# Optimization experiments

Hardware: AMD Instinct MI355X
Metric: run time of the kernel (lower is better)

Reference implementation:

```python
import jax, jax.numpy as jnp
import numpy as np

D_MODEL = 1024
NUM_HEADS = 16
D_K = D_MODEL // NUM_HEADS
B, L = 2, 2048


def setup_inputs() -> dict:
    key = jax.random.key(0)
    ks = jax.random.split(key, 10)
    s = 1.0 / np.sqrt(D_MODEL)
    inp = {
        "x": jax.random.normal(ks[0], (B, L, D_MODEL), dtype=jnp.float32),
        "mask": jnp.ones((B, L, L), dtype=jnp.int32),
        "wq": jax.random.uniform(ks[1], (D_MODEL, D_MODEL), jnp.float32, -s, s),
        "bq": jax.random.uniform(ks[2], (D_MODEL,), jnp.float32, -s, s),
        "wk": jax.random.uniform(ks[3], (D_MODEL, D_MODEL), jnp.float32, -s, s),
        "bk": jax.random.uniform(ks[4], (D_MODEL,), jnp.float32, -s, s),
        "wv": jax.random.uniform(ks[5], (D_MODEL, D_MODEL), jnp.float32, -s, s),
        "bv": jax.random.uniform(ks[6], (D_MODEL,), jnp.float32, -s, s),
        "wo": jax.random.uniform(ks[7], (D_MODEL, D_MODEL), jnp.float32, -s, s),
        "bo": jax.random.uniform(ks[8], (D_MODEL,), jnp.float32, -s, s),
    }
    return inp


def reference(x, mask, wq, bq, wk, bk, wv, bv, wo, bo):
    Bs, Ls, C = x.shape
    # linear projections, then split heads: [B, L, C] -> [B, h, L, d_k]
    def split_heads(t):
        return t.reshape(Bs, Ls, NUM_HEADS, D_K).transpose(0, 2, 1, 3)
    q = split_heads(x @ wq + bq)
    k = split_heads(x @ wk + bk)
    v = split_heads(x @ wv + bv)
    scores = jnp.einsum("bhlc,bhkc->bhlk", q, k) / np.sqrt(D_K)
    # mask: [B, L, L] -> [B, 1, L, L]; fill masked positions with -1e9
    scores = jnp.where(mask[:, None, :, :] == 0, jnp.float32(-1e9), scores)
    attn = jax.nn.softmax(scores, axis=-1)  # dropout p=0.0 -> identity
    out = jnp.einsum("bhlk,bhkc->bhlc", attn, v)
    out = out.transpose(0, 2, 1, 3).reshape(Bs, Ls, C)
    return out @ wo + bo
```

## Files before the change

kernel.cpp:

```cpp
#include <hip/hip_runtime.h>
#include <stdint.h>

#define D_MODEL 1024
#define NHEAD   16
#define DK      64
#define BATCH   2
#define SEQ     2048
#define MTOT    (BATCH*SEQ)

typedef unsigned short u16;
typedef unsigned int   u32;
typedef u16    u16x4  __attribute__((ext_vector_type(4)));
typedef u16    u16x8  __attribute__((ext_vector_type(8)));
typedef u32    u32x4  __attribute__((ext_vector_type(4)));
typedef __bf16 bf16x8 __attribute__((ext_vector_type(8)));
typedef float  f32x4  __attribute__((ext_vector_type(4)));
typedef float  f32x16 __attribute__((ext_vector_type(16)));

__device__ __forceinline__ u16 f2bf(float f) {
  union { float f; unsigned u; } v; v.f = f;
  return (u16)((v.u + 0x7fffu + ((v.u >> 16) & 1u)) >> 16);
}

__device__ __forceinline__ void gl_lds16(const void* g, void* l) {
  __builtin_amdgcn_global_load_lds((const __attribute__((address_space(1))) void*)g,
                                   (__attribute__((address_space(3))) void*)l, 16, 0, 0);
}

__device__ __forceinline__ bf16x8 ld_frag(const u16* p) {
  return __builtin_bit_cast(bf16x8, *(const u16x8*)p);
}

__device__ __forceinline__ u32 cvtpk(float lo, float hi) {
  u32 r;
  asm("v_cvt_pk_bf16_f32 %0, %1, %2" : "=v"(r) : "v"(lo), "v"(hi));
  return r;
}

__global__ __launch_bounds__(256) void k_cvt_x(const float* __restrict__ x, u16* __restrict__ xb) {
  int i = blockIdx.x * 256 + threadIdx.x;
  const float4 v = ((const float4*)x)[i];
  u16x4 o; o[0]=f2bf(v.x); o[1]=f2bf(v.y); o[2]=f2bf(v.z); o[3]=f2bf(v.w);
  *(u16x4*)(xb + (size_t)i*4) = o;
}

__global__ __launch_bounds__(256) void k_wtrans(const float* __restrict__ wq, const float* __restrict__ wk,
                                                const float* __restrict__ wv, const float* __restrict__ wo,
                                                u16* __restrict__ wqkv_t, u16* __restrict__ wo_t) {
  __shared__ float tile[32][33];
  const int z = blockIdx.z;
  const float* src = (z==0)?wq:(z==1)?wk:(z==2)?wv:wo;
  const int kb = blockIdx.y*32, nb = blockIdx.x*32;
  const int tx = threadIdx.x & 31, ty = threadIdx.x >> 5;
  #pragma unroll
  for (int i=0;i<4;i++)
    tile[ty + i*8][tx] = src[(size_t)(kb + ty + i*8)*D_MODEL + nb + tx];
  __syncthreads();
  u16* dst = (z<3) ? (wqkv_t + (size_t)z*D_MODEL*D_MODEL) : wo_t;
  #pragma unroll
  for (int i=0;i<4;i++) {
    int n = nb + ty + i*8, k = kb + tx;
    dst[(size_t)n*D_MODEL + k] = f2bf(tile[tx][ty + i*8]);
  }
}

__global__ __launch_bounds__(256) void k_maskpack(const int* __restrict__ mask,
                                                  unsigned long long* __restrict__ mb) {
  const int wid = blockIdx.x*4 + (threadIdx.x >> 6);
  const int lane = threadIdx.x & 63;
  for (int t2 = 0; t2 < 32; ++t2) {
    int word = wid*32 + t2;
    int row = word >> 5;
    int kb = word & 31;
    int m = mask[(size_t)row*SEQ + kb*64 + lane];
    unsigned long long bits = __ballot(m != 0);
    if (lane == 0) mb[word] = bits;
  }
}

__global__ __launch_bounds__(256) void k_vtrans(const u16* __restrict__ V, u16* __restrict__ Vt) {
  __shared__ u16 tile[64][72];
  const int bh = blockIdx.x >> 5;
  const int l0 = (blockIdx.x & 31) * 64;
  const int t = threadIdx.x;
  const u16* src = V + ((size_t)bh*SEQ + l0)*DK;
  #pragma unroll
  for (int j=0;j<2;j++) {
    int idx = t + j*256;
    int r = idx >> 3, c8 = (idx & 7)*8;
    *(u16x8*)&tile[r][c8] = *(const u16x8*)(src + (size_t)r*DK + c8);
  }
  __syncthreads();
  u16* dst = Vt + (size_t)bh*DK*SEQ + l0;
  #pragma unroll
  for (int j=0;j<2;j++) {
    int idx = t + j*256;
    int d = idx >> 3, k8 = (idx & 7)*8;
    u16x8 o;
    #pragma unroll
    for (int e=0;e<8;e++) o[e] = tile[k8 + e][d];
    *(u16x8*)(dst + (size_t)d*SEQ + k8) = o;
  }
}

template<int EPI>
__global__ __launch_bounds__(256) void k_gemm(const u16* __restrict__ A, const u16* __restrict__ Bt,
                                              const int M, const int N, const int K, const int nbm,
                                              const float* __restrict__ bq, const float* __restrict__ bk,
                                              const float* __restrict__ bv,
                                              u16* __restrict__ Qo, u16* __restrict__ Ko, u16* __restrict__ Vo,
                                              const float* __restrict__ bo, float* __restrict__ out) {
  __shared__ u16 As[128*32];
  __shared__ u16 Bs[128*32];
  const int t = threadIdx.x, lane = t & 63, w = t >> 6;
  const int bm = blockIdx.x % nbm, bn = blockIdx.x / nbm;
  const int brow = bm*128, bcol = bn*128;

  const int srow = w*32 + (lane >> 2);
  const int sswz = (lane & 3) ^ ((lane >> 2) & 3);
  const u16* aS0 = A  + (size_t)(brow + srow)*K + sswz*8;
  const u16* aS1 = aS0 + (size_t)16*K;
  const u16* bS0 = Bt + (size_t)(bcol + srow)*K + sswz*8;
  const u16* bS1 = bS0 + (size_t)16*K;
  u16* aD0 = As + w*1024; u16* aD1 = aD0 + 512;
  u16* bD0 = Bs + w*1024; u16* bD1 = bD0 + 512;

  const int wr = w >> 1, wc = w & 1;
  const int slotA = (lane >> 4) ^ (lane & 3);
  const u16* aRd = As + (wr*64 + (lane & 15))*32 + slotA*8;
  const u16* bRd = Bs + (wc*64 + (lane & 15))*32 + slotA*8;

  f32x4 acc[4][4];
  #pragma unroll
  for (int i=0;i<4;i++)
    #pragma unroll
    for (int j=0;j<4;j++) acc[i][j] = (f32x4){0.f,0.f,0.f,0.f};

  for (int kt = 0; kt < K; kt += 32) {
    gl_lds16(aS0 + kt, aD0);
    gl_lds16(aS1 + kt, aD1);
    gl_lds16(bS0 + kt, bD0);
    gl_lds16(bS1 + kt, bD1);
    __syncthreads();
    bf16x8 af[4], bfr[4];
    #pragma unroll
    for (int m=0;m<4;m++) af[m] = ld_frag(aRd + m*512);
    #pragma unroll
    for (int n=0;n<4;n++) bfr[n] = ld_frag(bRd + n*512);
    #pragma unroll
    for (int m=0;m<4;m++)
      #pragma unroll
      for (int n=0;n<4;n++)
        acc[m][n] = __builtin_amdgcn_mfma_f32_16x16x32_bf16(af[m], bfr[n], acc[m][n], 0,0,0);
    __syncthreads();
  }

  const int orow = brow + wr*64 + (lane >> 4)*4;
  const int ocol = bcol + wc*64 + (lane & 15);
  if (EPI == 0) {
    const int mat = ocol >> 10;
    const float* bias = (mat==0) ? bq : (mat==1) ? bk : bv;
    u16* outp = (mat==0) ? Qo : (mat==1) ? Ko : Vo;
    const float scal = (mat==0) ? 0.125f*1.4426950408889634f : 1.0f;
    #pragma unroll
    for (int m=0;m<4;m++) {
      #pragma unroll
      for (int n=0;n<4;n++) {
        int col = ocol + n*16;
        int c = col & 1023;
        float bb = bias[c];
        int h = c >> 6, d = c & 63;
        #pragma unroll
        for (int j=0;j<4;j++) {
          int row = orow + m*16 + j;
          int b = row >> 11, l = row & 2047;
          float v = (acc[m][n][j] + bb) * scal;
          outp[(((size_t)(b*NHEAD + h)*SEQ + l) << 6) + d] = f2bf(v);
        }
      }
    }
  } else {
    #pragma unroll
    for (int m=0;m<4;m++)
      #pragma unroll
      for (int n=0;n<4;n++) {
        int col = ocol + n*16;
        float bb = bo[col];
        #pragma unroll
        for (int j=0;j<4;j++) {
          int row = orow + m*16 + j;
          out[(size_t)row*N + col] = acc[m][n][j] + bb;
        }
      }
  }
}

__global__ __launch_bounds__(512, 4) void k_attn(const u16* __restrict__ Q, const u16* __restrict__ K,
                                                 const u16* __restrict__ Vt,
                                                 const unsigned long long* __restrict__ MB,
                                                 u16* __restrict__ AO) {
  __shared__ char smem[36864];
  const int t = threadIdx.x, lane = t & 63, w = t >> 6;
  const int hf = w >> 2, widx = w & 3;
  const int bid = blockIdx.x;
  const int swz = (bid & 7)*64 + (bid >> 3);
  const int bh = swz >> 4;
  const int q0 = (swz & 15) * 128;
  const int b = bh >> 4, h = bh & 15;
  const int lq = lane & 31, hi = lane >> 5, l7 = lane & 7;

  u16* Kbuf = (u16*)(smem + hf*16384);
  u16* Vbuf = (u16*)(smem + hf*16384 + 8192);

  const int qg = q0 + widx*32 + lq;
  const u16* qp = Q + ((size_t)bh*SEQ + qg)*DK + hi*8;
  bf16x8 qf[4];
  #pragma unroll
  for (int ks=0;ks<4;ks++) qf[ks] = ld_frag(qp + ks*16);

  const int srow = widx*16 + (lane >> 3);
  const int sswz = l7 ^ ((lane >> 3) & 7);
  const u16* kSb = K  + ((size_t)bh*SEQ + srow)*DK + sswz*8;
  const u16* vSb = Vt + ((size_t)bh*DK + srow)*SEQ + sswz*8;
  u16* kD0 = Kbuf + widx*1024; u16* kD1 = kD0 + 512;
  u16* vD0 = Vbuf + widx*1024; u16* vD1 = vD0 + 512;

  f32x16 o0 = 0.f, o1 = 0.f;
  float m_run = -1e30f, l_run = 0.f;
  const unsigned long long* mbp = MB + ((size_t)b*SEQ + qg)*32;

  for (int i = 0; i < 16; ++i) {
    const int ktg = hf*16 + i;
    const u16* kp = kSb + (size_t)ktg*64*DK;
    const u16* vp = vSb + ktg*64;
    gl_lds16(kp, kD0); gl_lds16(kp + 8*DK, kD1);
    gl_lds16(vp, vD0); gl_lds16(vp + 8*SEQ, vD1);
    __syncthreads();

    f32x16 s0 = 0.f, s1 = 0.f;
    #pragma unroll
    for (int ks=0;ks<4;ks++) {
      const int ph = (ks*2 + hi) ^ l7;
      bf16x8 kf0 = ld_frag(Kbuf + lq*64 + ph*8);
      bf16x8 kf1 = ld_frag(Kbuf + (32+lq)*64 + ph*8);
      s0 = __builtin_amdgcn_mfma_f32_32x32x16_bf16(kf0, qf[ks], s0, 0,0,0);
      s1 = __builtin_amdgcn_mfma_f32_32x32x16_bf16(kf1, qf[ks], s1, 0,0,0);
    }

    unsigned long long mb = mbp[ktg];
    if (!__all(mb == ~0ull)) {
      #pragma unroll
      for (int r=0;r<16;r++) {
        int kl = (r&3) + 8*(r>>2) + 4*hi;
        if (!((mb >> kl) & 1ull)) s0[r] = -1e9f;
        if (!((mb >> (kl+32)) & 1ull)) s1[r] = -1e9f;
      }
    }

    float tm[16];
    #pragma unroll
    for (int r=0;r<16;r++) tm[r] = fmaxf(s0[r], s1[r]);
    #pragma unroll
    for (int st=8; st>0; st>>=1)
      #pragma unroll
      for (int r=0;r<8;r++) if (r < st) tm[r] = fmaxf(tm[r], tm[r+st]);
    float mx = fmaxf(tm[0], __shfl_xor(tm[0], 32));
    if (!__all(mx <= m_run + 8.0f)) {
      float m_new = fmaxf(m_run, mx);
      float corr = __builtin_amdgcn_exp2f(m_run - m_new);
      l_run *= corr;
      #pragma unroll
      for (int r=0;r<16;r++) { o0[r] *= corr; o1[r] *= corr; }
      m_run = m_new;
    }
    float ts[16];
    #pragma unroll
    for (int r=0;r<16;r++) {
      s0[r] = __builtin_amdgcn_exp2f(s0[r] - m_run);
      s1[r] = __builtin_amdgcn_exp2f(s1[r] - m_run);
      ts[r] = s0[r] + s1[r];
    }
    #pragma unroll
    for (int st=8; st>0; st>>=1)
      #pragma unroll
      for (int r=0;r<8;r++) if (r < st) ts[r] += ts[r+st];
    l_run += ts[0] + __shfl_xor(ts[0], 32);

    #pragma unroll
    for (int kt2=0;kt2<2;kt2++) {
      const f32x16& sv = kt2 ? s1 : s0;
      u32 w0 = cvtpk(sv[0],  sv[1]),  w1 = cvtpk(sv[2],  sv[3]);
      u32 w2 = cvtpk(sv[4],  sv[5]),  w3 = cvtpk(sv[6],  sv[7]);
      u32 w4 = cvtpk(sv[8],  sv[9]),  w5 = cvtpk(sv[10], sv[11]);
      u32 w6 = cvtpk(sv[12], sv[13]), w7 = cvtpk(sv[14], sv[15]);
      asm volatile("v_permlane32_swap_b32 %0, %1" : "+v"(w0), "+v"(w2));
      asm volatile("v_permlane32_swap_b32 %0, %1" : "+v"(w1), "+v"(w3));
      asm volatile("v_permlane32_swap_b32 %0, %1" : "+v"(w4), "+v"(w6));
      asm volatile("v_permlane32_swap_b32 %0, %1" : "+v"(w5), "+v"(w7));
      bf16x8 pa0 = __builtin_bit_cast(bf16x8, (u32x4){w0, w1, w2, w3});
      bf16x8 pa1 = __builtin_bit_cast(bf16x8, (u32x4){w4, w5, w6, w7});
      const int ph0 = ((kt2*2+0)*2 + hi) ^ l7;
      const int ph1 = ((kt2*2+1)*2 + hi) ^ l7;
      bf16x8 v00 = ld_frag(Vbuf + lq*64      + ph0*8);
      bf16x8 v01 = ld_frag(Vbuf + lq*64      + ph1*8);
      bf16x8 v10 = ld_frag(Vbuf + (32+lq)*64 + ph0*8);
      bf16x8 v11 = ld_frag(Vbuf + (32+lq)*64 + ph1*8);
      o0 = __builtin_amdgcn_mfma_f32_32x32x16_bf16(v00, pa0, o0, 0,0,0);
      o0 = __builtin_amdgcn_mfma_f32_32x32x16_bf16(v01, pa1, o0, 0,0,0);
      o1 = __builtin_amdgcn_mfma_f32_32x32x16_bf16(v10, pa0, o1, 0,0,0);
      o1 = __builtin_amdgcn_mfma_f32_32x32x16_bf16(v11, pa1, o1, 0,0,0);
    }
    __syncthreads();
  }

  float* marea = (float*)smem;
  if (hf == 1) {
    float* p = marea + (size_t)(widx*64 + lane)*35;
    #pragma unroll
    for (int r=0;r<16;r++) { p[r] = o0[r]; p[16+r] = o1[r]; }
    p[32] = m_run; p[33] = l_run;
  }
  __syncthreads();
  if (hf == 0) {
    const float* p = marea + (size_t)(widx*64 + lane)*35;
    float m1 = p[32], l1 = p[33];
    float mm = fmaxf(m_run, m1);
    float c0 = __builtin_amdgcn_exp2f(m_run - mm);
    float c1 = __builtin_amdgcn_exp2f(m1 - mm);
    float inv = 1.0f / (l_run*c0 + l1*c1);
    size_t base = ((size_t)(b*SEQ + qg))*D_MODEL + h*DK;
    u16x4 g;
    #pragma unroll
    for (int rr=0;rr<4;rr++) {
      #pragma unroll
      for (int i2=0;i2<4;i2++) g[i2] = f2bf((o0[rr*4+i2]*c0 + p[rr*4+i2]*c1) * inv);
      *(u16x4*)(AO + base + rr*8 + hi*4) = g;
    }
    #pragma unroll
    for (int rr=0;rr<4;rr++) {
      #pragma unroll
      for (int i2=0;i2<4;i2++) g[i2] = f2bf((o1[rr*4+i2]*c0 + p[16+rr*4+i2]*c1) * inv);
      *(u16x4*)(AO + base + 32 + rr*8 + hi*4) = g;
    }
  }
}

extern "C" void kernel_launch(void* const* d_in, const int* in_sizes, int n_in,
                              void* d_out, int out_size, void* d_ws, size_t ws_size,
                              hipStream_t stream) {
  const float* x  = (const float*)d_in[0];
  const int*  msk = (const int*)d_in[1];
  const float* wq = (const float*)d_in[2];
  const float* bq = (const float*)d_in[3];
  const float* wk = (const float*)d_in[4];
  const float* bk = (const float*)d_in[5];
  const float* wv = (const float*)d_in[6];
  const float* bv = (const float*)d_in[7];
  const float* wo = (const float*)d_in[8];
  const float* bo = (const float*)d_in[9];
  float* out = (float*)d_out;

  char* ws = (char*)d_ws;
  size_t off = 0;
  u16* Xb   = (u16*)(ws + off); off += (size_t)MTOT*D_MODEL*2;
  u16* Wqkv = (u16*)(ws + off); off += (size_t)3*D_MODEL*D_MODEL*2;
  u16* Wot  = (u16*)(ws + off); off += (size_t)D_MODEL*D_MODEL*2;
  u16* Qb   = (u16*)(ws + off); off += (size_t)BATCH*NHEAD*SEQ*DK*2;
  u16* Kb   = (u16*)(ws + off); off += (size_t)BATCH*NHEAD*SEQ*DK*2;
  u16* Vb   = (u16*)(ws + off); off += (size_t)BATCH*NHEAD*SEQ*DK*2;
  u16* Vtb  = (u16*)(ws + off); off += (size_t)BATCH*NHEAD*SEQ*DK*2;
  u16* AO   = (u16*)(ws + off); off += (size_t)MTOT*D_MODEL*2;
  unsigned long long* Mb = (unsigned long long*)(ws + off);

  k_cvt_x<<<MTOT*D_MODEL/4/256, 256, 0, stream>>>(x, Xb);
  k_wtrans<<<dim3(32,32,4), 256, 0, stream>>>(wq, wk, wv, wo, Wqkv, Wot);
  k_maskpack<<<1024, 256, 0, stream>>>(msk, Mb);
  k_gemm<0><<<(MTOT/128)*(3*D_MODEL/128), 256, 0, stream>>>(
      Xb, Wqkv, MTOT, 3*D_MODEL, D_MODEL, MTOT/128,
      bq, bk, bv, Qb, Kb, Vb, nullptr, nullptr);
  k_vtrans<<<BATCH*NHEAD*(SEQ/64), 256, 0, stream>>>(Vb, Vtb);
  k_attn<<<BATCH*NHEAD*(SEQ/128), 512, 0, stream>>>(Qb, Kb, Vtb, Mb, AO);
  k_gemm<1><<<(MTOT/128)*(D_MODEL/128), 256, 0, stream>>>(
      AO, Wot, MTOT, D_MODEL, D_MODEL, MTOT/128,
      nullptr, nullptr, nullptr, nullptr, nullptr, nullptr, bo, out);
}
```

Measured before the change: 151.7 us.

## Double-buffer K/V tiles in LDS and split softmax into 32-key sub-blocks

The attention kernel now double-buffers K and V tiles in LDS, prefetching the next tile with async global-to-LDS loads while the current one is computed. This replaces the two per-iteration __syncthreads with a single waitcnt plus barrier. The 64-key tile is now handled as two 32-key sub-blocks with an online softmax update per sub-block, which lowers register pressure. MFMA sections are wrapped in s_setprio. LDS use grows from 36KB to 64KB per block, which cuts blocks per CU and may hurt occupancy against launch_bounds(512,4).

```diff
diff --git a/kernel.cpp b/kernel.cpp
--- a/kernel.cpp
+++ b/kernel.cpp
@@ -199,7 +199,7 @@
                                                  const u16* __restrict__ Vt,
                                                  const unsigned long long* __restrict__ MB,
                                                  u16* __restrict__ AO) {
-  __shared__ char smem[36864];
+  __shared__ char smem[65536];
   const int t = threadIdx.x, lane = t & 63, w = t >> 6;
   const int hf = w >> 2, widx = w & 3;
   const int bid = blockIdx.x;
@@ -209,9 +209,6 @@
   const int b = bh >> 4, h = bh & 15;
   const int lq = lane & 31, hi = lane >> 5, l7 = lane & 7;
 
-  u16* Kbuf = (u16*)(smem + hf*16384);
-  u16* Vbuf = (u16*)(smem + hf*16384 + 8192);
-
   const int qg = q0 + widx*32 + lq;
   const u16* qp = Q + ((size_t)bh*SEQ + qg)*DK + hi*8;
   bf16x8 qf[4];
@@ -222,96 +219,107 @@
   const int sswz = l7 ^ ((lane >> 3) & 7);
   const u16* kSb = K  + ((size_t)bh*SEQ + srow)*DK + sswz*8;
   const u16* vSb = Vt + ((size_t)bh*DK + srow)*SEQ + sswz*8;
-  u16* kD0 = Kbuf + widx*1024; u16* kD1 = kD0 + 512;
-  u16* vD0 = Vbuf + widx*1024; u16* vD1 = vD0 + 512;
 
   f32x16 o0 = 0.f, o1 = 0.f;
   float m_run = -1e30f, l_run = 0.f;
   const unsigned long long* mbp = MB + ((size_t)b*SEQ + qg)*32;
 
+  #define STAGE(buf, tile) do {                                           \
+    const u16* kp_ = kSb + (size_t)(tile)*64*DK;                          \
+    const u16* vp_ = vSb + (size_t)(tile)*64;                             \
+    u16* kd_ = (u16*)(smem + (buf)*32768 + hf*16384) + widx*1024;         \
+    u16* vd_ = (u16*)(smem + (buf)*32768 + hf*16384 + 8192) + widx*1024;  \
+    gl_lds16(kp_, kd_); gl_lds16(kp_ + 8*DK, kd_ + 512);                  \
+    gl_lds16(vp_, vd_); gl_lds16(vp_ + 8*SEQ, vd_ + 512);                 \
+  } while (0)
+
+  STAGE(0, hf*16);
+  asm volatile("s_waitcnt vmcnt(0)" ::: "memory");
+  __builtin_amdgcn_s_barrier();
+
   for (int i = 0; i < 16; ++i) {
-    const int ktg = hf*16 + i;
-    const u16* kp = kSb + (size_t)ktg*64*DK;
-    const u16* vp = vSb + ktg*64;
-    gl_lds16(kp, kD0); gl_lds16(kp + 8*DK, kD1);
-    gl_lds16(vp, vD0); gl_lds16(vp + 8*SEQ, vD1);
-    __syncthreads();
-
-    f32x16 s0 = 0.f, s1 = 0.f;
-    #pragma unroll
-    for (int ks=0;ks<4;ks++) {
-      const int ph = (ks*2 + hi) ^ l7;
-      bf16x8 kf0 = ld_frag(Kbuf + lq*64 + ph*8);
-      bf16x8 kf1 = ld_frag(Kbuf + (32+lq)*64 + ph*8);
-      s0 = __builtin_amdgcn_mfma_f32_32x32x16_bf16(kf0, qf[ks], s0, 0,0,0);
-      s1 = __builtin_amdgcn_mfma_f32_32x32x16_bf16(kf1, qf[ks], s1, 0,0,0);
-    }
-
-    unsigned long long mb = mbp[ktg];
-    if (!__all(mb == ~0ull)) {
-      #pragma unroll
-      for (int r=0;r<16;r++) {
-        int kl = (r&3) + 8*(r>>2) + 4*hi;
-        if (!((mb >> kl) & 1ull)) s0[r] = -1e9f;
-        if (!((mb >> (kl+32)) & 1ull)) s1[r] = -1e9f;
-      }
-    }
-
-    float tm[16];
-    #pragma unroll
-    for (int r=0;r<16;r++) tm[r] = fmaxf(s0[r], s1[r]);
-    #pragma unroll
-    for (int st=8; st>0; st>>=1)
-      #pragma unroll
-      for (int r=0;r<8;r++) if (r < st) tm[r] = fmaxf(tm[r], tm[r+st]);
-    float mx = fmaxf(tm[0], __shfl_xor(tm[0], 32));
-    if (!__all(mx <= m_run + 8.0f)) {
-      float m_new = fmaxf(m_run, mx);
-      float corr = __builtin_amdgcn_exp2f(m_run - m_new);
-      l_run *= corr;
-      #pragma unroll
-      for (int r=0;r<16;r++) { o0[r] *= corr; o1[r] *= corr; }
-      m_run = m_new;
-    }
-    float ts[16];
-    #pragma unroll
-    for (int r=0;r<16;r++) {
-      s0[r] = __builtin_amdgcn_exp2f(s0[r] - m_run);
-      s1[r] = __builtin_amdgcn_exp2f(s1[r] - m_run);
-      ts[r] = s0[r] + s1[r];
-    }
-    #pragma unroll
-    for (int st=8; st>0; st>>=1)
-      #pragma unroll
-      for (int r=0;r<8;r++) if (r < st) ts[r] += ts[r+st];
-    l_run += ts[0] + __shfl_xor(ts[0], 32);
-
-    #pragma unroll
-    for (int kt2=0;kt2<2;kt2++) {
-      const f32x16& sv = kt2 ? s1 : s0;
-      u32 w0 = cvtpk(sv[0],  sv[1]),  w1 = cvtpk(sv[2],  sv[3]);
-      u32 w2 = cvtpk(sv[4],  sv[5]),  w3 = cvtpk(sv[6],  sv[7]);
-      u32 w4 = cvtpk(sv[8],  sv[9]),  w5 = cvtpk(sv[10], sv[11]);
-      u32 w6 = cvtpk(sv[12], sv[13]), w7 = cvtpk(sv[14], sv[15]);
+    const int cur = i & 1;
+    if (i + 1 < 16) STAGE(cur ^ 1, hf*16 + i + 1);
+    const u16* Kbuf = (const u16*)(smem + cur*32768 + hf*16384);
+    const u16* Vbuf = (const u16*)(smem + cur*32768 + hf*16384 + 8192);
+    const unsigned long long mb = mbp[hf*16 + i];
+    const bool full = __all(mb == ~0ull);
+
+    #pragma unroll
+    for (int sub = 0; sub < 2; ++sub) {
+      f32x16 s = 0.f;
+      __builtin_amdgcn_s_setprio(1);
+      #pragma unroll
+      for (int ks=0;ks<4;ks++) {
+        const int ph = (ks*2 + hi) ^ l7;
+        bf16x8 kf = ld_frag(Kbuf + (sub*32 + lq)*64 + ph*8);
+        s = __builtin_amdgcn_mfma_f32_32x32x16_bf16(kf, qf[ks], s, 0,0,0);
+      }
+      __builtin_amdgcn_s_setprio(0);
+
+      if (!full) {
+        #pragma unroll
+        for (int r=0;r<16;r++) {
+          int kl = sub*32 + (r&3) + 8*(r>>2) + 4*hi;
+          if (!((mb >> kl) & 1ull)) s[r] = -1e9f;
+        }
+      }
+
+      float tm[8];
+      #pragma unroll
+      for (int r=0;r<8;r++) tm[r] = fmaxf(s[r], s[8+r]);
+      #pragma unroll
+      for (int st=4; st>0; st>>=1)
+        #pragma unroll
+        for (int r=0;r<4;r++) if (r < st) tm[r] = fmaxf(tm[r], tm[r+st]);
+      float mx = fmaxf(tm[0], __shfl_xor(tm[0], 32));
+      if (!__all(mx <= m_run + 8.0f)) {
+        float m_new = fmaxf(m_run, mx);
+        float corr = __builtin_amdgcn_exp2f(m_run - m_new);
+        l_run *= corr;
+        #pragma unroll
+        for (int r=0;r<16;r++) { o0[r] *= corr; o1[r] *= corr; }
+        m_run = m_new;
+      }
+      #pragma unroll
+      for (int r=0;r<16;r++) s[r] = __builtin_amdgcn_exp2f(s[r] - m_run);
+      float ts[8];
+      #pragma unroll
+      for (int r=0;r<8;r++) ts[r] = s[r] + s[8+r];
+      #pragma unroll
+      for (int st=4; st>0; st>>=1)
+        #pragma unroll
+        for (int r=0;r<4;r++) if (r < st) ts[r] += ts[r+st];
+      l_run += ts[0] + __shfl_xor(ts[0], 32);
+
+      u32 w0 = cvtpk(s[0],  s[1]),  w1 = cvtpk(s[2],  s[3]);
+      u32 w2 = cvtpk(s[4],  s[5]),  w3 = cvtpk(s[6],  s[7]);
+      u32 w4 = cvtpk(s[8],  s[9]),  w5 = cvtpk(s[10], s[11]);
+      u32 w6 = cvtpk(s[12], s[13]), w7 = cvtpk(s[14], s[15]);
       asm volatile("v_permlane32_swap_b32 %0, %1" : "+v"(w0), "+v"(w2));
       asm volatile("v_permlane32_swap_b32 %0, %1" : "+v"(w1), "+v"(w3));
       asm volatile("v_permlane32_swap_b32 %0, %1" : "+v"(w4), "+v"(w6));
       asm volatile("v_permlane32_swap_b32 %0, %1" : "+v"(w5), "+v"(w7));
       bf16x8 pa0 = __builtin_bit_cast(bf16x8, (u32x4){w0, w1, w2, w3});
       bf16x8 pa1 = __builtin_bit_cast(bf16x8, (u32x4){w4, w5, w6, w7});
-      const int ph0 = ((kt2*2+0)*2 + hi) ^ l7;
-      const int ph1 = ((kt2*2+1)*2 + hi) ^ l7;
+      const int ph0 = ((sub*2+0)*2 + hi) ^ l7;
+      const int ph1 = ((sub*2+1)*2 + hi) ^ l7;
       bf16x8 v00 = ld_frag(Vbuf + lq*64      + ph0*8);
       bf16x8 v01 = ld_frag(Vbuf + lq*64      + ph1*8);
       bf16x8 v10 = ld_frag(Vbuf + (32+lq)*64 + ph0*8);
       bf16x8 v11 = ld_frag(Vbuf + (32+lq)*64 + ph1*8);
+      __builtin_amdgcn_s_setprio(1);
       o0 = __builtin_amdgcn_mfma_f32_32x32x16_bf16(v00, pa0, o0, 0,0,0);
       o0 = __builtin_amdgcn_mfma_f32_32x32x16_bf16(v01, pa1, o0, 0,0,0);
       o1 = __builtin_amdgcn_mfma_f32_32x32x16_bf16(v10, pa0, o1, 0,0,0);
       o1 = __builtin_amdgcn_mfma_f32_32x32x16_bf16(v11, pa1, o1, 0,0,0);
+      __builtin_amdgcn_s_setprio(0);
     }
-    __syncthreads();
-  }
+
+    asm volatile("s_waitcnt vmcnt(0)" ::: "memory");
+    __builtin_amdgcn_s_barrier();
+  }
+  #undef STAGE
 
   float* marea = (float*)smem;
   if (hf == 1) {
```

Measured after the change: 150.5 us. Within noise of the previous version (-0.8%).
